# Performance work log

Measured on AMD Instinct MI355X. Metric: run time of the kernel, lower is better.

Reference implementation:

```python
import jax, jax.numpy as jnp
import numpy as np

S = 4096  # source_sequence_size
Q = 4096  # query_sequence_size
E = 2048  # embedding_size
D = 2048  # output_embedding_size


def setup_inputs() -> dict:
    key = jax.random.key(0)
    ks = jax.random.split(key, 9)
    s = 1.0 / np.sqrt(E)
    return {
        "key": jax.random.normal(ks[0], (S, E), jnp.float32),
        "value": jax.random.normal(ks[1], (S, E), jnp.float32),
        "query": jax.random.normal(ks[2], (Q, E), jnp.float32),
        "Wk": jax.random.normal(ks[3], (D, E), jnp.float32) * s,
        "bk": jax.random.normal(ks[4], (D,), jnp.float32) * 0.01,
        "Wq": jax.random.normal(ks[5], (D, E), jnp.float32) * s,
        "bq": jax.random.normal(ks[6], (D,), jnp.float32) * 0.01,
        "Wv": jax.random.normal(ks[7], (D, E), jnp.float32) * s,
        "bv": jax.random.normal(ks[8], (D,), jnp.float32) * 0.01,
    }


def reference(key, value, query, Wk, bk, Wq, bq, Wv, bv):
    # Linear projections (nn.Linear: x @ W.T + b)
    k = key @ Wk.T + bk      # [S, D]
    v = value @ Wv.T + bv    # [S, D]
    q = query @ Wq.T + bq    # [Q, D]
    # Per-query-token attention scores over all source tokens (schema BOTH),
    # then weighted sum over value rows -- vectorized form of the per-token
    # apply_attention_scores loop.
    scale = 1.0 / jnp.sqrt(jnp.asarray(D, q.dtype))
    scores = jax.nn.softmax(jnp.einsum("qd,sd->qs", q, k) * scale, axis=-1)  # [Q, S]
    return jnp.einsum("qs,sd->qd", scores, v)  # [Q, D]
```

## Files before the change

### kernel.cpp

```cpp
#include <hip/hip_runtime.h>

#define S_SEQ 4096
#define Q_SEQ 4096
#define E_DIM 2048
#define D_DIM 2048

typedef __bf16 bf16;
typedef __bf16 bf16x4 __attribute__((ext_vector_type(4)));
typedef __bf16 bf16x8 __attribute__((ext_vector_type(8)));
typedef float f32x4 __attribute__((ext_vector_type(4)));

__global__ __launch_bounds__(256) void cast6(
    const float* __restrict__ i0, const float* __restrict__ i1,
    const float* __restrict__ i2, const float* __restrict__ i3,
    const float* __restrict__ i4, const float* __restrict__ i5,
    bf16* __restrict__ o0, bf16* __restrict__ o1, bf16* __restrict__ o2,
    bf16* __restrict__ o3, bf16* __restrict__ o4, bf16* __restrict__ o5) {
  const float* in;
  bf16* out;
  int n4;
  switch (blockIdx.y) {
    case 0: in = i0; out = o0; n4 = (S_SEQ * E_DIM) / 4; break;
    case 1: in = i1; out = o1; n4 = (S_SEQ * E_DIM) / 4; break;
    case 2: in = i2; out = o2; n4 = (S_SEQ * E_DIM) / 4; break;
    case 3: in = i3; out = o3; n4 = (D_DIM * E_DIM) / 4; break;
    case 4: in = i4; out = o4; n4 = (D_DIM * E_DIM) / 4; break;
    default: in = i5; out = o5; n4 = (D_DIM * E_DIM) / 4; break;
  }
  int i = blockIdx.x * 256 + threadIdx.x;
  if (i < n4) {
    float4 v = reinterpret_cast<const float4*>(in)[i];
    bf16x4 o;
    o[0] = (bf16)v.x; o[1] = (bf16)v.y; o[2] = (bf16)v.z; o[3] = (bf16)v.w;
    *reinterpret_cast<bf16x4*>(out + 4 * (size_t)i) = o;
  }
}

__device__ __forceinline__ void async_copy16(const bf16* g, bf16* l) {
  __builtin_amdgcn_global_load_lds(
      (const __attribute__((address_space(1))) void*)g,
      (__attribute__((address_space(3))) void*)l, 16, 0, 0);
}

__device__ __forceinline__ void xcd_remap(int id, int nt, int& m, int& n) {
  int xcd = id & 7;
  int lid = id >> 3;
  m = (xcd & 3) * 8 + (lid & 7);
  n = (xcd >> 2) * (nt >> 1) + (lid >> 3);
}

template <int EPI>
__device__ __forceinline__ void gemm_body(
    const bf16* __restrict__ A, int lda,
    const bf16* __restrict__ B, int ldb,
    void* __restrict__ C, int ldc,
    const float* __restrict__ aux, float scale, int K, int mBase, int nBase) {
  __shared__ __align__(16) bf16 Als[128 * 64];
  __shared__ __align__(16) bf16 Bls[128 * 64];

  const int tid  = threadIdx.x;
  const int wave = tid >> 6;
  const int lane = tid & 63;
  const int quad = lane >> 4;
  const int lrow = lane & 15;
  const int wRow = (wave >> 1) * 64;
  const int wCol = (wave & 1) * 64;

  f32x4 acc[4][4];
#pragma unroll
  for (int i = 0; i < 4; ++i)
#pragma unroll
    for (int j = 0; j < 4; ++j) {
      f32x4 z = {0.f, 0.f, 0.f, 0.f};
      acc[i][j] = z;
    }

  for (int k0 = 0; k0 < K; k0 += 64) {
#pragma unroll
    for (int c = 0; c < 4; ++c) {
      int chunk = c * 256 + tid;
      int row = chunk >> 3;
      int kc = (chunk & 7) ^ (row & 7);
      const bf16* g = A + (size_t)(mBase + row) * lda + k0 + kc * 8;
      async_copy16(g, Als + (size_t)(c * 256 + wave * 64) * 8);
    }
#pragma unroll
    for (int c = 0; c < 4; ++c) {
      int chunk = c * 256 + tid;
      int row = chunk >> 3;
      int kc = (chunk & 7) ^ (row & 7);
      const bf16* g = B + (size_t)(nBase + row) * ldb + k0 + kc * 8;
      async_copy16(g, Bls + (size_t)(c * 256 + wave * 64) * 8);
    }
    __syncthreads();

#pragma unroll
    for (int kk = 0; kk < 2; ++kk) {
      bf16x8 af[4], bfr[4];
#pragma unroll
      for (int i = 0; i < 4; ++i) {
        int r = wRow + i * 16 + lrow;
        int slot = (kk * 4 + quad) ^ (r & 7);
        af[i] = *(const bf16x8*)(Als + (size_t)r * 64 + slot * 8);
      }
#pragma unroll
      for (int j = 0; j < 4; ++j) {
        int r = wCol + j * 16 + lrow;
        int slot = (kk * 4 + quad) ^ (r & 7);
        bfr[j] = *(const bf16x8*)(Bls + (size_t)r * 64 + slot * 8);
      }
#pragma unroll
      for (int i = 0; i < 4; ++i)
#pragma unroll
        for (int j = 0; j < 4; ++j)
          acc[i][j] = __builtin_amdgcn_mfma_f32_16x16x32_bf16(af[i], bfr[j], acc[i][j], 0, 0, 0);
    }
    __syncthreads();
  }

  float rinv[4][4];
  if (EPI == 2) {
#pragma unroll
    for (int i = 0; i < 4; ++i)
#pragma unroll
      for (int r = 0; r < 4; ++r)
        rinv[i][r] = aux[mBase + wRow + i * 16 + quad * 4 + r];
  }
#pragma unroll
  for (int j = 0; j < 4; ++j) {
    const int cn = nBase + wCol + j * 16 + lrow;
    float bj = 0.f;
    if (EPI == 0) bj = aux[cn];
#pragma unroll
    for (int i = 0; i < 4; ++i) {
      const int rbase = mBase + wRow + i * 16 + quad * 4;
#pragma unroll
      for (int r = 0; r < 4; ++r) {
        if (EPI == 0)
          ((bf16*)C)[(size_t)(rbase + r) * ldc + cn] = (bf16)(acc[i][j][r] + bj);
        else if (EPI == 1)
          ((bf16*)C)[(size_t)(rbase + r) * ldc + cn] =
              (bf16)__expf(acc[i][j][r] * scale);
        else
          ((float*)C)[(size_t)(rbase + r) * ldc + cn] = acc[i][j][r] * rinv[i][r];
      }
    }
  }
}

__global__ __launch_bounds__(256, 2) void qk_gemm(
    const bf16* __restrict__ A, const bf16* __restrict__ B,
    bf16* __restrict__ E, float scale) {
  int m, n;
  xcd_remap(blockIdx.x, 32, m, n);
  gemm_body<1>(A, D_DIM, B, D_DIM, (void*)E, S_SEQ, nullptr, scale, D_DIM,
               m * 128, n * 128);
}

__global__ __launch_bounds__(256, 2) void pv_gemm(
    const bf16* __restrict__ E, const bf16* __restrict__ vT,
    float* __restrict__ out, const float* __restrict__ inv) {
  int m, n;
  xcd_remap(blockIdx.x, 16, m, n);
  gemm_body<2>(E, S_SEQ, vT, S_SEQ, (void*)out, D_DIM, inv, 0.f, S_SEQ,
               m * 128, n * 128);
}

__global__ __launch_bounds__(256, 2) void proj_gemm(
    const bf16* __restrict__ xk, const bf16* __restrict__ xq,
    const bf16* __restrict__ xv,
    const bf16* __restrict__ Wk, const bf16* __restrict__ Wq,
    const bf16* __restrict__ Wv,
    const float* __restrict__ bk, const float* __restrict__ bq,
    const float* __restrict__ bv,
    bf16* __restrict__ ok, bf16* __restrict__ oq, bf16* __restrict__ ov) {
  const bf16 *A, *W;
  const float* b;
  bf16* o;
  switch (blockIdx.z) {
    case 0: A = xk; W = Wk; b = bk; o = ok; break;
    case 1: A = xq; W = Wq; b = bq; o = oq; break;
    default: A = xv; W = Wv; b = bv; o = ov; break;
  }
  int m, n;
  xcd_remap(blockIdx.x, 16, m, n);
  gemm_body<0>(A, E_DIM, W, E_DIM, (void*)o, D_DIM, b, 0.f, E_DIM,
               m * 128, n * 128);
}

__global__ __launch_bounds__(256) void transpose_bf16(
    const bf16* __restrict__ in, bf16* __restrict__ out) {
  __shared__ bf16 tile[64][66];
  const int t = threadIdx.x;
  const int c0 = blockIdx.x * 64;
  const int r0 = blockIdx.y * 64;
  const int col = t & 63;
  const int r4 = t >> 6;
#pragma unroll
  for (int i = 0; i < 16; ++i) {
    int rr = i * 4 + r4;
    tile[rr][col] = in[(size_t)(r0 + rr) * D_DIM + c0 + col];
  }
  __syncthreads();
#pragma unroll
  for (int i = 0; i < 16; ++i) {
    int rr = i * 4 + r4;
    out[(size_t)(c0 + rr) * S_SEQ + r0 + col] = tile[col][rr];
  }
}

__global__ __launch_bounds__(256) void rowsum_inv(
    const bf16* __restrict__ E, float* __restrict__ inv) {
  const int t = threadIdx.x;
  const int wave = t >> 6;
  const int lane = t & 63;
  const int row = blockIdx.x * 4 + wave;
  const bf16x8* src = (const bf16x8*)(E + (size_t)row * S_SEQ);
  float s = 0.f;
#pragma unroll
  for (int i = 0; i < 8; ++i) {
    bf16x8 v = src[lane + i * 64];
#pragma unroll
    for (int j = 0; j < 8; ++j) s += (float)v[j];
  }
#pragma unroll
  for (int off = 32; off > 0; off >>= 1)
    s += __shfl_down(s, off, 64);
  if (lane == 0) inv[row] = 1.0f / s;
}

extern "C" void kernel_launch(void* const* d_in, const int* in_sizes, int n_in,
                              void* d_out, int out_size, void* d_ws, size_t ws_size,
                              hipStream_t stream) {
  const float* key   = (const float*)d_in[0];
  const float* value = (const float*)d_in[1];
  const float* query = (const float*)d_in[2];
  const float* Wk = (const float*)d_in[3];
  const float* bk = (const float*)d_in[4];
  const float* Wq = (const float*)d_in[5];
  const float* bq = (const float*)d_in[6];
  const float* Wv = (const float*)d_in[7];
  const float* bv = (const float*)d_in[8];

  const size_t MB = 1ull << 20;
  char* ws = (char*)d_ws;
  bf16* key_bf   = (bf16*)(ws + 0 * MB);
  bf16* value_bf = (bf16*)(ws + 16 * MB);
  bf16* query_bf = (bf16*)(ws + 32 * MB);
  bf16* Wk_bf    = (bf16*)(ws + 48 * MB);
  bf16* Wq_bf    = (bf16*)(ws + 56 * MB);
  bf16* Wv_bf    = (bf16*)(ws + 64 * MB);
  bf16* k_bf     = (bf16*)(ws + 72 * MB);
  bf16* q_bf     = (bf16*)(ws + 88 * MB);
  bf16* v_bf     = (bf16*)(ws + 104 * MB);
  bf16* vT_bf    = (bf16*)(ws + 120 * MB);
  bf16* E        = (bf16*)(ws + 0 * MB);
  float* inv     = (float*)(ws + 34 * MB);

  dim3 blk(256);

  cast6<<<dim3(8192, 6), blk, 0, stream>>>(
      key, value, query, Wk, Wq, Wv,
      key_bf, value_bf, query_bf, Wk_bf, Wq_bf, Wv_bf);

  proj_gemm<<<dim3(512, 1, 3), blk, 0, stream>>>(
      key_bf, query_bf, value_bf, Wk_bf, Wq_bf, Wv_bf, bk, bq, bv,
      k_bf, q_bf, v_bf);

  transpose_bf16<<<dim3(D_DIM / 64, S_SEQ / 64), blk, 0, stream>>>(v_bf, vT_bf);

  const float scale = 0.022097086912079608f;
  qk_gemm<<<dim3(1024), blk, 0, stream>>>(q_bf, k_bf, E, scale);

  rowsum_inv<<<dim3(1024), blk, 0, stream>>>(E, inv);

  pv_gemm<<<dim3(512), blk, 0, stream>>>(E, vT_bf, (float*)d_out, inv);
}
```

Baseline: 427.6 us.

## Restructure GEMMs into 256x128 tiles with 8 waves and double-buffered ping-pong pipeline

Rewrites the shared GEMM body to use 512-thread blocks on 256x128 output tiles with double-buffered LDS. Global-to-LDS async loads are split into half-tiles and interleaved with MFMA phases, gated by explicit vmcnt/lgkmcnt waits, barriers and setprio. The goal is to hide memory latency behind matrix math and raise reuse per block, and the XCD remap and grid sizes are adjusted to match. The hand-scheduled barriers and waitcnt values add correctness risk, and the larger LDS footprint may lower occupancy.

```diff
diff --git a/kernel.cpp b/kernel.cpp
--- a/kernel.cpp
+++ b/kernel.cpp
@@ -45,9 +45,46 @@
 __device__ __forceinline__ void xcd_remap(int id, int nt, int& m, int& n) {
   int xcd = id & 7;
   int lid = id >> 3;
-  m = (xcd & 3) * 8 + (lid & 7);
-  n = (xcd >> 2) * (nt >> 1) + (lid >> 3);
-}
+  m = (xcd & 3) * 4 + (lid & 3);
+  n = (xcd >> 2) * (nt >> 1) + (lid >> 2);
+}
+
+__device__ __forceinline__ void stage_half(const bf16* __restrict__ G, int ld,
+                                           int grow0, int k0, bf16* lds,
+                                           int wave, int lane) {
+#pragma unroll
+  for (int s = 0; s < 2; ++s) {
+    int c = (wave * 2 + s) * 64 + lane;
+    int row = c >> 3;
+    int kc = (c & 7) ^ (row & 7);
+    const bf16* g = G + (size_t)(grow0 + row) * ld + k0 + kc * 8;
+    async_copy16(g, lds + (size_t)(wave * 2 + s) * 512);
+  }
+}
+
+#define BARRIER __builtin_amdgcn_s_barrier()
+#define LGKM0 asm volatile("s_waitcnt lgkmcnt(0)" ::: "memory")
+#define VMCNT4 asm volatile("s_waitcnt vmcnt(4)" ::: "memory")
+#define VMCNT0 asm volatile("s_waitcnt vmcnt(0)" ::: "memory")
+
+#define RD_A(buf, IP)                                                         \
+  _Pragma("unroll") for (int ii = 0; ii < 2; ++ii)                            \
+  _Pragma("unroll") for (int kk = 0; kk < 2; ++kk)                            \
+      aR[ii][kk] = *(const bf16x8*)(&Als[buf][(size_t)(wRow + ((IP)*2 + ii) * 16 + lrow) * 64 + slotk[kk] * 8]);
+
+#define RD_B(buf, JP, dst)                                                    \
+  _Pragma("unroll") for (int jj = 0; jj < 2; ++jj)                            \
+  _Pragma("unroll") for (int kk = 0; kk < 2; ++kk)                            \
+      dst[jj][kk] = *(const bf16x8*)(&Bls[buf][(size_t)(wCol + ((JP)*2 + jj) * 16 + lrow) * 64 + slotk[kk] * 8]);
+
+#define MMA(IP, JP, bsrc)                                                     \
+  __builtin_amdgcn_s_setprio(1);                                              \
+  _Pragma("unroll") for (int ii = 0; ii < 2; ++ii)                            \
+  _Pragma("unroll") for (int jj = 0; jj < 2; ++jj)                            \
+  _Pragma("unroll") for (int kk = 0; kk < 2; ++kk)                            \
+      acc[(IP)*2 + ii][(JP)*2 + jj] = __builtin_amdgcn_mfma_f32_16x16x32_bf16( \
+          aR[ii][kk], bsrc[jj][kk], acc[(IP)*2 + ii][(JP)*2 + jj], 0, 0, 0);  \
+  __builtin_amdgcn_s_setprio(0)
 
 template <int EPI>
 __device__ __forceinline__ void gemm_body(
@@ -55,8 +92,8 @@
     const bf16* __restrict__ B, int ldb,
     void* __restrict__ C, int ldc,
     const float* __restrict__ aux, float scale, int K, int mBase, int nBase) {
-  __shared__ __align__(16) bf16 Als[128 * 64];
-  __shared__ __align__(16) bf16 Bls[128 * 64];
+  __shared__ __align__(16) bf16 Als[2][256 * 64];
+  __shared__ __align__(16) bf16 Bls[2][128 * 64];
 
   const int tid  = threadIdx.x;
   const int wave = tid >> 6;
@@ -65,6 +102,7 @@
   const int lrow = lane & 15;
   const int wRow = (wave >> 1) * 64;
   const int wCol = (wave & 1) * 64;
+  const int slotk[2] = {quad ^ (lrow & 7), (4 + quad) ^ (lrow & 7)};
 
   f32x4 acc[4][4];
 #pragma unroll
@@ -75,47 +113,51 @@
       acc[i][j] = z;
     }
 
-  for (int k0 = 0; k0 < K; k0 += 64) {
-#pragma unroll
-    for (int c = 0; c < 4; ++c) {
-      int chunk = c * 256 + tid;
-      int row = chunk >> 3;
-      int kc = (chunk & 7) ^ (row & 7);
-      const bf16* g = A + (size_t)(mBase + row) * lda + k0 + kc * 8;
-      async_copy16(g, Als + (size_t)(c * 256 + wave * 64) * 8);
+  bf16x8 aR[2][2], b0[2][2], b1[2][2];
+
+  stage_half(B, ldb, nBase, 0, &Bls[0][0], wave, lane);
+  stage_half(A, lda, mBase, 0, &Als[0][0], wave, lane);
+  stage_half(A, lda, mBase + 128, 0, &Als[0][128 * 64], wave, lane);
+  stage_half(B, ldb, nBase, 64, &Bls[1][0], wave, lane);
+  stage_half(A, lda, mBase, 64, &Als[1][0], wave, lane);
+  VMCNT4;
+  BARRIER;
+
+  const int NI = K >> 7;
+#pragma unroll 1
+  for (int i = 0; i < NI; ++i) {
+    const bool nl = (i + 1 < NI);
+    const int kb = i * 128;
+    RD_A(0, 0);
+    RD_B(0, 0, b0);
+    stage_half(A, lda, mBase + 128, kb + 64, &Als[1][128 * 64], wave, lane);
+    BARRIER; LGKM0; MMA(0, 0, b0); BARRIER;
+    RD_B(0, 1, b1);
+    BARRIER; LGKM0; MMA(0, 1, b1); BARRIER;
+    RD_A(0, 1);
+    if (nl) stage_half(B, ldb, nBase, kb + 128, &Bls[0][0], wave, lane);
+    BARRIER; LGKM0; MMA(1, 1, b1); BARRIER;
+    if (nl) {
+      stage_half(A, lda, mBase, kb + 128, &Als[0][0], wave, lane);
+      VMCNT4;
+    } else {
+      VMCNT0;
     }
-#pragma unroll
-    for (int c = 0; c < 4; ++c) {
-      int chunk = c * 256 + tid;
-      int row = chunk >> 3;
-      int kc = (chunk & 7) ^ (row & 7);
-      const bf16* g = B + (size_t)(nBase + row) * ldb + k0 + kc * 8;
-      async_copy16(g, Bls + (size_t)(c * 256 + wave * 64) * 8);
+    BARRIER; LGKM0; MMA(1, 0, b0); BARRIER;
+    RD_A(1, 0);
+    RD_B(1, 0, b0);
+    if (nl) stage_half(A, lda, mBase + 128, kb + 128, &Als[0][128 * 64], wave, lane);
+    BARRIER; LGKM0; MMA(0, 0, b0); BARRIER;
+    RD_B(1, 1, b1);
+    BARRIER; LGKM0; MMA(0, 1, b1); BARRIER;
+    RD_A(1, 1);
+    if (nl) stage_half(B, ldb, nBase, kb + 192, &Bls[1][0], wave, lane);
+    BARRIER; LGKM0; MMA(1, 1, b1); BARRIER;
+    if (nl) {
+      stage_half(A, lda, mBase, kb + 192, &Als[1][0], wave, lane);
+      VMCNT4;
     }
-    __syncthreads();
-
-#pragma unroll
-    for (int kk = 0; kk < 2; ++kk) {
-      bf16x8 af[4], bfr[4];
-#pragma unroll
-      for (int i = 0; i < 4; ++i) {
-        int r = wRow + i * 16 + lrow;
-        int slot = (kk * 4 + quad) ^ (r & 7);
-        af[i] = *(const bf16x8*)(Als + (size_t)r * 64 + slot * 8);
-      }
-#pragma unroll
-      for (int j = 0; j < 4; ++j) {
-        int r = wCol + j * 16 + lrow;
-        int slot = (kk * 4 + quad) ^ (r & 7);
-        bfr[j] = *(const bf16x8*)(Bls + (size_t)r * 64 + slot * 8);
-      }
-#pragma unroll
-      for (int i = 0; i < 4; ++i)
-#pragma unroll
-        for (int j = 0; j < 4; ++j)
-          acc[i][j] = __builtin_amdgcn_mfma_f32_16x16x32_bf16(af[i], bfr[j], acc[i][j], 0, 0, 0);
-    }
-    __syncthreads();
+    BARRIER; LGKM0; MMA(1, 0, b0); BARRIER;
   }
 
   float rinv[4][4];
@@ -148,25 +190,25 @@
   }
 }
 
-__global__ __launch_bounds__(256, 2) void qk_gemm(
+__global__ __launch_bounds__(512, 2) void qk_gemm(
     const bf16* __restrict__ A, const bf16* __restrict__ B,
     bf16* __restrict__ E, float scale) {
   int m, n;
   xcd_remap(blockIdx.x, 32, m, n);
   gemm_body<1>(A, D_DIM, B, D_DIM, (void*)E, S_SEQ, nullptr, scale, D_DIM,
-               m * 128, n * 128);
-}
-
-__global__ __launch_bounds__(256, 2) void pv_gemm(
+               m * 256, n * 128);
+}
+
+__global__ __launch_bounds__(512, 2) void pv_gemm(
     const bf16* __restrict__ E, const bf16* __restrict__ vT,
     float* __restrict__ out, const float* __restrict__ inv) {
   int m, n;
   xcd_remap(blockIdx.x, 16, m, n);
   gemm_body<2>(E, S_SEQ, vT, S_SEQ, (void*)out, D_DIM, inv, 0.f, S_SEQ,
-               m * 128, n * 128);
-}
-
-__global__ __launch_bounds__(256, 2) void proj_gemm(
+               m * 256, n * 128);
+}
+
+__global__ __launch_bounds__(512, 2) void proj_gemm(
     const bf16* __restrict__ xk, const bf16* __restrict__ xq,
     const bf16* __restrict__ xv,
     const bf16* __restrict__ Wk, const bf16* __restrict__ Wq,
@@ -185,7 +227,7 @@
   int m, n;
   xcd_remap(blockIdx.x, 16, m, n);
   gemm_body<0>(A, E_DIM, W, E_DIM, (void*)o, D_DIM, b, 0.f, E_DIM,
-               m * 128, n * 128);
+               m * 256, n * 128);
 }
 
 __global__ __launch_bounds__(256) void transpose_bf16(
@@ -258,21 +300,22 @@
   float* inv     = (float*)(ws + 34 * MB);
 
   dim3 blk(256);
+  dim3 blk512(512);
 
   cast6<<<dim3(8192, 6), blk, 0, stream>>>(
       key, value, query, Wk, Wq, Wv,
       key_bf, value_bf, query_bf, Wk_bf, Wq_bf, Wv_bf);
 
-  proj_gemm<<<dim3(512, 1, 3), blk, 0, stream>>>(
+  proj_gemm<<<dim3(256, 1, 3), blk512, 0, stream>>>(
       key_bf, query_bf, value_bf, Wk_bf, Wq_bf, Wv_bf, bk, bq, bv,
       k_bf, q_bf, v_bf);
 
   transpose_bf16<<<dim3(D_DIM / 64, S_SEQ / 64), blk, 0, stream>>>(v_bf, vT_bf);
 
   const float scale = 0.022097086912079608f;
-  qk_gemm<<<dim3(1024), blk, 0, stream>>>(q_bf, k_bf, E, scale);
+  qk_gemm<<<dim3(512), blk512, 0, stream>>>(q_bf, k_bf, E, scale);
 
   rowsum_inv<<<dim3(1024), blk, 0, stream>>>(E, inv);
 
-  pv_gemm<<<dim3(512), blk, 0, stream>>>(E, vT_bf, (float*)d_out, inv);
-}
+  pv_gemm<<<dim3(256), blk512, 0, stream>>>(E, vT_bf, (float*)d_out, inv);
+}
```

New measurement: 471.8 us. +10.3%, slower.
